# Performance work log

Measured on AMD Instinct MI355X. Metric: run time of the kernel, lower is better.

Reference implementation:

```python
import jax, jax.numpy as jnp
import numpy as np

K = 128      # knowledge_n
E = 4096     # exer_n
S = 2048     # student_n
M = 512      # number of supervised exercises (ex_id)
NUM_UPDATE = 3
THRESHOLD = 0.05
H = 1.0


def setup_inputs() -> dict:
    key = jax.random.key(0)
    ks = jax.random.split(key, 16)
    U_embeding = jax.random.uniform(ks[0], (S, K), dtype=jnp.float32)
    W = jax.random.uniform(ks[1], (K, E), dtype=jnp.float32)
    beiTa_1 = jax.random.uniform(ks[2], (K, E), dtype=jnp.float32)
    beiTa_2 = jax.random.uniform(ks[3], (E, 1), dtype=jnp.float32)
    B = jax.random.uniform(ks[4], (K, E, K), dtype=jnp.float32)
    guess_slip = jax.random.normal(ks[5], (E, 2), dtype=jnp.float32)
    A_emb = jax.random.normal(ks[6], (E, 3), dtype=jnp.float32)
    gamma_c = jax.random.normal(ks[7], (E, 1), dtype=jnp.float32)
    gamma_e = jax.random.normal(ks[8], (E, 1), dtype=jnp.float32)
    alpha = jax.random.normal(ks[9], (E, 1), dtype=jnp.float32)
    score = jax.random.randint(ks[10], (E, 1), 0, 2).astype(jnp.float32)
    user_k_kc = (jax.random.uniform(ks[11], (K, E)) < 0.3).astype(jnp.float32)
    # multi-hot question->concept map, ~4 concepts per exercise, at least 1
    q_kn = (jax.random.uniform(ks[12], (E, K)) < 4.0 / K).astype(jnp.float32)
    q_kn = q_kn.at[jnp.arange(E), jax.random.randint(ks[13], (E,), 0, K)].set(1.0)
    d = q_kn.sum(axis=1, keepdims=True)  # exercise degree, >= 1
    ex_id = jax.random.randint(ks[14], (M,), 0, E, dtype=jnp.int32)
    kn_id = jnp.arange(K, dtype=jnp.int32)
    stu_id = 7
    return dict(U_embeding=U_embeding, W=W, beiTa_1=beiTa_1, beiTa_2=beiTa_2,
                B=B, guess_slip=guess_slip, A_emb=A_emb, gamma_c=gamma_c,
                gamma_e=gamma_e, alpha=alpha, score=score, user_k_kc=user_k_kc,
                q_kn=q_kn, d=d, stu_id=stu_id, kn_id=kn_id, ex_id=ex_id)


def reference(U_embeding, W, beiTa_1, beiTa_2, B, guess_slip, A_emb,
              gamma_c, gamma_e, alpha, score, user_k_kc, q_kn, d,
              stu_id, kn_id, ex_id):
    # The torch loop `for cur_kn in kn_id: update(cur_kn, U_update[num-1])` is a
    # Jacobi sweep: every concept update reads the PREVIOUS state, so all
    # concepts can be computed in one vectorized pass per iteration.
    Bdiag = jnp.einsum('kek->ke', B)           # B[k, e, k], (K, E)
    dvec = d[:, 0]                              # (E,)
    sc = score[:, 0]                            # (E,)
    upd = jnp.zeros((K,), dtype=bool).at[kn_id].set(True)

    def step(u):                                # u: (K,) current mastery state
        # ---- Ic (eq. 7): per-exercise interaction term ----
        su = q_kn @ u                           # (E,)  sum of mastered concepts
        yc = jnp.exp(-(sc - su / dvec) ** 2)    # (E,)
        Pc = jnp.concatenate([1.0 - guess_slip, yc[:, None]], axis=1)  # (E,3)
        Ic = jax.nn.sigmoid(-jnp.sum(A_emb * Pc, axis=1))              # (E,)
        # ---- Gkc: masked, dead-zoned neighbour influence ----
        # U_gkc entries with q_kn==0 are set to 0.5, and column cur_kn is
        # zeroed; dead-zone of 0.5 contributes 0, so it reduces to a gated
        # product with the k-diagonal term subtracted out.
        dv = jnp.where(jnp.abs(u - 0.5) > THRESHOLD, u - 0.5, 0.0)      # (K,)
        qdv = q_kn * dv                         # (E, K)
        Gsum = jnp.einsum('kej,ej->ke', B, qdv) - Bdiag * qdv.T         # (K, E)
        # NOTE: the original subtracts 0.5 twice (sigmoid(...) - 0.5 then
        # reshape(...) - 0.5); replicated faithfully.
        Gkc = jax.nn.sigmoid(-Gsum) - 1.0       # (K, E)
        # ---- Zc ----
        Zc = jax.nn.sigmoid(-(gamma_c[:, 0] / dvec) * (sc - 0.5)) - 0.5  # (E,)
        # ---- WKC and the per-concept contraction over the exercise set ----
        WK = H * Ic[None, :] * (beiTa_1 * Gkc + (beiTa_2[:, 0] * Zc)[None, :])
        s = jnp.sum(user_k_kc * W * WK, axis=1)  # ragged set via 0/1 mask, (K,)
        u_new = jax.nn.sigmoid(-s)
        return jnp.where(upd, u_new, u)

    u0 = U_embeding[stu_id]                     # (K,)
    states = [u0]
    diffs = []
    for _ in range(NUM_UPDATE):
        un = step(states[-1])
        diffs.append(jnp.linalg.norm(un - states[-1]))
        states.append(un)

    state_last = states[-1][:, None]            # U_update[-2] in torch indexing
    state_2nd_last = states[-2][:, None]        # U_update[-3]
    diff_norm = jnp.stack(diffs)

    # ---- supervised predict ----
    Ukse = (q_kn[ex_id] @ state_last) / d[ex_id] - 0.5                  # (M,1)
    predict = jax.nn.sigmoid(-(alpha[ex_id] * Ukse + gamma_e[ex_id]))   # (M,1)
    return (state_last, state_2nd_last, predict, diff_norm)
```

## Files before the change

kernel.cpp:

```cpp
#include <hip/hip_runtime.h>
#include <math.h>

#define KK 128
#define EE 4096
#define MM 512
#define MAXNZ 32

#define OFF_PART 128
#define OFF_CNT  2176
#define OFF_IDX  6272
#define OFF_PE   137344

__global__ __launch_bounds__(256) void k_setup(
    const float* __restrict__ U, const float* __restrict__ beiTa_2,
    const float* __restrict__ guess_slip, const float* __restrict__ A_emb,
    const float* __restrict__ gamma_c, const float* __restrict__ score,
    const float* __restrict__ q_kn, const float* __restrict__ d,
    const int* __restrict__ stu_id, float* __restrict__ ws)
{
    int e = blockIdx.x * 256 + threadIdx.x;
    int* cnt = (int*)(ws + OFF_CNT);
    int* idx = (int*)(ws + OFF_IDX);
    float* P01  = ws + OFF_PE;
    float* a2   = P01 + EE;
    float* scv  = a2 + EE;
    float* invd = scv + EE;
    float* bz   = invd + EE;

    const float4* qrow = (const float4*)(q_kn + (size_t)e * KK);
    int c = 0;
    for (int j4 = 0; j4 < KK / 4; j4++) {
        float4 q = qrow[j4];
        int j = j4 * 4;
        if (q.x > 0.5f) { if (c < MAXNZ) idx[e * MAXNZ + c] = j;     c++; }
        if (q.y > 0.5f) { if (c < MAXNZ) idx[e * MAXNZ + c] = j + 1; c++; }
        if (q.z > 0.5f) { if (c < MAXNZ) idx[e * MAXNZ + c] = j + 2; c++; }
        if (q.w > 0.5f) { if (c < MAXNZ) idx[e * MAXNZ + c] = j + 3; c++; }
    }
    cnt[e] = (c < MAXNZ) ? c : MAXNZ;

    float id_ = 1.0f / d[e];
    invd[e] = id_;
    float scr = score[e];
    scv[e] = scr;
    P01[e] = A_emb[3 * e] * (1.0f - guess_slip[2 * e]) +
             A_emb[3 * e + 1] * (1.0f - guess_slip[2 * e + 1]);
    a2[e] = A_emb[3 * e + 2];
    float zc = 1.0f / (1.0f + __expf(gamma_c[e] * id_ * (scr - 0.5f))) - 0.5f;
    bz[e] = beiTa_2[e] * zc;

    if (blockIdx.x == 0 && threadIdx.x < KK) {
        ws[threadIdx.x] = U[(size_t)stu_id[0] * KK + threadIdx.x];
    }
}

__global__ __launch_bounds__(256) void k_iter(
    const float* __restrict__ B, const float* __restrict__ W,
    const float* __restrict__ beiTa_1, const float* __restrict__ ukc,
    float* __restrict__ ws)
{
    __shared__ float lu[KK];
    __shared__ float ldv[KK];
    __shared__ float red[256];
    int tid = threadIdx.x;
    int k = blockIdx.y;
    int e = blockIdx.x * 256 + tid;

    if (tid < KK) {
        float uv = ws[tid];
        lu[tid] = uv;
        float t = uv - 0.5f;
        ldv[tid] = (fabsf(t) > 0.05f) ? t : 0.0f;
    }
    __syncthreads();

    const int* cnt = (const int*)(ws + OFF_CNT);
    const int* ip  = (const int*)(ws + OFF_IDX) + e * MAXNZ;
    const float* P01  = ws + OFF_PE;
    const float* a2   = P01 + EE;
    const float* scv  = a2 + EE;
    const float* invd = scv + EE;
    const float* bz   = invd + EE;

    int c = cnt[e];
    const float* Brow = B + ((size_t)k * EE + (size_t)e) * KK;
    float su = 0.0f, gs = 0.0f;
    for (int i = 0; i < c; i++) {
        int j = ip[i];
        su += lu[j];
        float dvj = ldv[j];
        if (j != k && dvj != 0.0f) gs += Brow[j] * dvj;
    }
    float t0 = scv[e] - su * invd[e];
    float yc = __expf(-t0 * t0);
    float Ic  = 1.0f / (1.0f + __expf(P01[e] + a2[e] * yc));
    float Gkc = 1.0f / (1.0f + __expf(gs)) - 1.0f;
    size_t o = (size_t)k * EE + (size_t)e;
    float WKv = Ic * (beiTa_1[o] * Gkc + bz[e]);
    float contrib = ukc[o] * W[o] * WKv;

    red[tid] = contrib;
    __syncthreads();
    for (int s2 = 128; s2 > 0; s2 >>= 1) {
        if (tid < s2) red[tid] += red[tid + s2];
        __syncthreads();
    }
    if (tid == 0) ws[OFF_PART + k * 16 + blockIdx.x] = red[0];
}

__global__ __launch_bounds__(128) void k_update(float* __restrict__ ws,
                                                float* __restrict__ out, int iter)
{
    __shared__ float red[KK];
    int k = threadIdx.x;
    float s = 0.0f;
    for (int t = 0; t < 16; t++) s += ws[OFF_PART + k * 16 + t];
    float un = 1.0f / (1.0f + __expf(s));
    float uo = ws[k];
    float dd = un - uo;
    red[k] = dd * dd;
    __syncthreads();
    for (int s2 = 64; s2 > 0; s2 >>= 1) {
        if (k < s2) red[k] += red[k + s2];
        __syncthreads();
    }
    if (k == 0) out[768 + iter] = sqrtf(red[0]);
    ws[k] = un;
    if (iter == 1) out[128 + k] = un;
}

__global__ __launch_bounds__(512) void k_final(
    float* __restrict__ ws, float* __restrict__ out,
    const int* __restrict__ ex_id, const float* __restrict__ alpha,
    const float* __restrict__ gamma_e)
{
    __shared__ float un_s[KK];
    __shared__ float red[KK];
    int tid = threadIdx.x;
    if (tid < KK) {
        float s = 0.0f;
        for (int t = 0; t < 16; t++) s += ws[OFF_PART + tid * 16 + t];
        float un = 1.0f / (1.0f + __expf(s));
        float uo = ws[tid];
        float dd = un - uo;
        red[tid] = dd * dd;
        un_s[tid] = un;
        out[tid] = un;
    }
    __syncthreads();
    for (int s2 = 64; s2 > 0; s2 >>= 1) {
        if (tid < s2) red[tid] += red[tid + s2];
        __syncthreads();
    }
    if (tid == 0) out[770] = sqrtf(red[0]);

    const int* cnt = (const int*)(ws + OFF_CNT);
    const int* idx = (const int*)(ws + OFF_IDX);
    const float* invd = ws + OFF_PE + 3 * EE;
    int e = ex_id[tid];
    int c = cnt[e];
    const int* ip = idx + e * MAXNZ;
    float su = 0.0f;
    for (int i = 0; i < c; i++) su += un_s[ip[i]];
    float Ukse = su * invd[e] - 0.5f;
    float p = 1.0f / (1.0f + __expf(alpha[e] * Ukse + gamma_e[e]));
    out[256 + tid] = p;
}

extern "C" void kernel_launch(void* const* d_in, const int* in_sizes, int n_in,
                              void* d_out, int out_size, void* d_ws, size_t ws_size,
                              hipStream_t stream) {
    const float* U          = (const float*)d_in[0];
    const float* W          = (const float*)d_in[1];
    const float* beiTa_1    = (const float*)d_in[2];
    const float* beiTa_2    = (const float*)d_in[3];
    const float* B          = (const float*)d_in[4];
    const float* guess_slip = (const float*)d_in[5];
    const float* A_emb      = (const float*)d_in[6];
    const float* gamma_c    = (const float*)d_in[7];
    const float* gamma_e    = (const float*)d_in[8];
    const float* alpha      = (const float*)d_in[9];
    const float* score      = (const float*)d_in[10];
    const float* ukc        = (const float*)d_in[11];
    const float* q_kn       = (const float*)d_in[12];
    const float* d          = (const float*)d_in[13];
    const int*   stu_id     = (const int*)d_in[14];
    const int*   ex_id      = (const int*)d_in[16];
    float* out = (float*)d_out;
    float* ws  = (float*)d_ws;

    k_setup<<<16, 256, 0, stream>>>(U, beiTa_2, guess_slip, A_emb, gamma_c,
                                    score, q_kn, d, stu_id, ws);
    for (int iter = 0; iter < 3; iter++) {
        k_iter<<<dim3(16, 128), 256, 0, stream>>>(B, W, beiTa_1, ukc, ws);
        if (iter < 2) {
            k_update<<<1, 128, 0, stream>>>(ws, out, iter);
        } else {
            k_final<<<1, 512, 0, stream>>>(ws, out, ex_id, alpha, gamma_e);
        }
    }
}
```

Measured before the change: 500.6 us.

## Compact sparse B entries once, then run later sweeps on compacted transposed data

Result: slower. 698.3 us (+39.5%).

```diff
diff --git a/kernel.cpp b/kernel.cpp
--- a/kernel.cpp
+++ b/kernel.cpp
@@ -4,129 +4,244 @@
 #define KK 128
 #define EE 4096
 #define MM 512
-#define MAXNZ 32
-
-#define OFF_PART 128
-#define OFF_CNT  2176
-#define OFF_IDX  6272
-#define OFF_PE   137344
+#define CP 32
+
+#define OFF_U    0
+#define OFF_P0   128
+#define OFF_P1   (128 + 4096)
+#define OFF_CNT  20608
+#define OFF_IDX  24704
+#define OFF_PE   155776
+#define OFF_UWT  180352
+#define OFF_B1T  704640
+#define OFF_BC   1228928
 
 __global__ __launch_bounds__(256) void k_setup(
-    const float* __restrict__ U, const float* __restrict__ beiTa_2,
+    const float* __restrict__ U, const float* __restrict__ W,
+    const float* __restrict__ beiTa_1, const float* __restrict__ beiTa_2,
     const float* __restrict__ guess_slip, const float* __restrict__ A_emb,
     const float* __restrict__ gamma_c, const float* __restrict__ score,
-    const float* __restrict__ q_kn, const float* __restrict__ d,
-    const int* __restrict__ stu_id, float* __restrict__ ws)
-{
-    int e = blockIdx.x * 256 + threadIdx.x;
-    int* cnt = (int*)(ws + OFF_CNT);
-    int* idx = (int*)(ws + OFF_IDX);
-    float* P01  = ws + OFF_PE;
-    float* a2   = P01 + EE;
-    float* scv  = a2 + EE;
-    float* invd = scv + EE;
-    float* bz   = invd + EE;
-
-    const float4* qrow = (const float4*)(q_kn + (size_t)e * KK);
-    int c = 0;
-    for (int j4 = 0; j4 < KK / 4; j4++) {
-        float4 q = qrow[j4];
-        int j = j4 * 4;
-        if (q.x > 0.5f) { if (c < MAXNZ) idx[e * MAXNZ + c] = j;     c++; }
-        if (q.y > 0.5f) { if (c < MAXNZ) idx[e * MAXNZ + c] = j + 1; c++; }
-        if (q.z > 0.5f) { if (c < MAXNZ) idx[e * MAXNZ + c] = j + 2; c++; }
-        if (q.w > 0.5f) { if (c < MAXNZ) idx[e * MAXNZ + c] = j + 3; c++; }
-    }
-    cnt[e] = (c < MAXNZ) ? c : MAXNZ;
-
-    float id_ = 1.0f / d[e];
-    invd[e] = id_;
-    float scr = score[e];
-    scv[e] = scr;
-    P01[e] = A_emb[3 * e] * (1.0f - guess_slip[2 * e]) +
-             A_emb[3 * e + 1] * (1.0f - guess_slip[2 * e + 1]);
-    a2[e] = A_emb[3 * e + 2];
-    float zc = 1.0f / (1.0f + __expf(gamma_c[e] * id_ * (scr - 0.5f))) - 0.5f;
-    bz[e] = beiTa_2[e] * zc;
-
-    if (blockIdx.x == 0 && threadIdx.x < KK) {
-        ws[threadIdx.x] = U[(size_t)stu_id[0] * KK + threadIdx.x];
-    }
-}
-
-__global__ __launch_bounds__(256) void k_iter(
-    const float* __restrict__ B, const float* __restrict__ W,
-    const float* __restrict__ beiTa_1, const float* __restrict__ ukc,
+    const float* __restrict__ ukc, const float* __restrict__ q_kn,
+    const float* __restrict__ d, const int* __restrict__ stu_id,
     float* __restrict__ ws)
 {
-    __shared__ float lu[KK];
-    __shared__ float ldv[KK];
-    __shared__ float red[256];
-    int tid = threadIdx.x;
-    int k = blockIdx.y;
-    int e = blockIdx.x * 256 + tid;
-
+    int tid = threadIdx.x;
+    int blk = blockIdx.x;
+    if (blk < 16) {
+        int e = blk * 256 + tid;
+        int* cnt = (int*)(ws + OFF_CNT);
+        int* idx = (int*)(ws + OFF_IDX);
+        float* P01  = ws + OFF_PE;
+        float* a2   = P01 + EE;
+        float* scv  = a2 + EE;
+        float* invd = scv + EE;
+        float* bz   = invd + EE;
+        float* Icv  = bz + EE;
+
+        const float4* qrow = (const float4*)(q_kn + (size_t)e * KK);
+        int c = 0;
+        for (int j4 = 0; j4 < KK / 4; j4++) {
+            float4 q = qrow[j4];
+            int j = j4 * 4;
+            if (q.x > 0.5f) { if (c < CP) idx[e * CP + c] = j;     c++; }
+            if (q.y > 0.5f) { if (c < CP) idx[e * CP + c] = j + 1; c++; }
+            if (q.z > 0.5f) { if (c < CP) idx[e * CP + c] = j + 2; c++; }
+            if (q.w > 0.5f) { if (c < CP) idx[e * CP + c] = j + 3; c++; }
+        }
+        c = (c < CP) ? c : CP;
+        cnt[e] = c;
+
+        float id_ = 1.0f / d[e];
+        invd[e] = id_;
+        float scr = score[e];
+        scv[e] = scr;
+        float p01 = A_emb[3 * e] * (1.0f - guess_slip[2 * e]) +
+                    A_emb[3 * e + 1] * (1.0f - guess_slip[2 * e + 1]);
+        P01[e] = p01;
+        float a2v = A_emb[3 * e + 2];
+        a2[e] = a2v;
+        float zc = 1.0f / (1.0f + __expf(gamma_c[e] * id_ * (scr - 0.5f))) - 0.5f;
+        bz[e] = beiTa_2[e] * zc;
+
+        const float* u0p = U + (size_t)stu_id[0] * KK;
+        float su = 0.0f;
+        for (int i = 0; i < c; i++) su += u0p[idx[e * CP + i]];
+        float t0 = scr - su * id_;
+        float yc = __expf(-t0 * t0);
+        Icv[e] = 1.0f / (1.0f + __expf(p01 + a2v * yc));
+
+        if (blk == 0 && tid < KK) ws[tid] = u0p[tid];
+    } else {
+        float* uWt = ws + OFF_UWT;
+        float* b1t = ws + OFF_B1T;
+        for (int t = (blk - 16) * 256 + tid; t < KK * EE; t += 48 * 256) {
+            int e = t >> 7;
+            int k = t & (KK - 1);
+            size_t src = (size_t)k * EE + e;
+            uWt[t] = ukc[src] * W[src];
+            b1t[t] = beiTa_1[src];
+        }
+    }
+}
+
+__global__ __launch_bounds__(256) void k_dense(
+    const float* __restrict__ B, const float* __restrict__ q_kn,
+    const float* __restrict__ W, const float* __restrict__ beiTa_1,
+    const float* __restrict__ ukc, float* __restrict__ ws)
+{
+    __shared__ float sdv[KK];
+    int tid = threadIdx.x;
     if (tid < KK) {
         float uv = ws[tid];
-        lu[tid] = uv;
         float t = uv - 0.5f;
-        ldv[tid] = (fabsf(t) > 0.05f) ? t : 0.0f;
-    }
-    __syncthreads();
+        sdv[tid] = (fabsf(t) > 0.05f) ? t : 0.0f;
+    }
+    __syncthreads();
+
+    int w    = blockIdx.x * 4 + (tid >> 6);
+    int lane = tid & 63;
+    int k    = w >> 5;
+    int ec   = w & 31;
+    int half = lane >> 5;
+    int ll   = lane & 31;
+    int j0   = ll * 4;
+
+    float dvm0 = (j0     != k) ? sdv[j0]     : 0.0f;
+    float dvm1 = (j0 + 1 != k) ? sdv[j0 + 1] : 0.0f;
+    float dvm2 = (j0 + 2 != k) ? sdv[j0 + 2] : 0.0f;
+    float dvm3 = (j0 + 3 != k) ? sdv[j0 + 3] : 0.0f;
+
+    const float* bzv = ws + OFF_PE + 4 * EE;
+    const float* Icv = ws + OFF_PE + 5 * EE;
+    float* Bc = ws + OFF_BC;
+    unsigned long long Lmask = (ll ? ((1ull << ll) - 1ull) : 0ull) << (half * 32);
+
+    float acc = 0.0f;
+    int ebase = ec * 128;
+    for (int ee = 0; ee < 128; ee += 2) {
+        int e = ebase + ee + half;
+        const float4 bq = *(const float4*)(q_kn + (size_t)e * KK + j0);
+        const float4 bb = *(const float4*)(B + ((size_t)k * EE + e) * KK + j0);
+
+        float p = bb.x * (bq.x * dvm0) + bb.y * (bq.y * dvm1) +
+                  bb.z * (bq.z * dvm2) + bb.w * (bq.w * dvm3);
+
+        bool f0 = bq.x > 0.5f, f1 = bq.y > 0.5f, f2 = bq.z > 0.5f, f3 = bq.w > 0.5f;
+        unsigned long long m0 = __ballot(f0), m1 = __ballot(f1);
+        unsigned long long m2 = __ballot(f2), m3 = __ballot(f3);
+        int i0 = __popcll(m0 & Lmask) + __popcll(m1 & Lmask) +
+                 __popcll(m2 & Lmask) + __popcll(m3 & Lmask);
+        int i1 = i0 + (f0 ? 1 : 0);
+        int i2 = i1 + (f1 ? 1 : 0);
+        int i3 = i2 + (f2 ? 1 : 0);
+        size_t bcb = (size_t)e * CP * KK + k;
+        if (f0 && i0 < CP) Bc[bcb + (size_t)i0 * KK] = bb.x;
+        if (f1 && i1 < CP) Bc[bcb + (size_t)i1 * KK] = bb.y;
+        if (f2 && i2 < CP) Bc[bcb + (size_t)i2 * KK] = bb.z;
+        if (f3 && i3 < CP) Bc[bcb + (size_t)i3 * KK] = bb.w;
+
+        for (int m = 1; m <= 16; m <<= 1) p += __shfl_xor(p, m, 32);
+
+        if (ll == 0) {
+            float Gkc = 1.0f / (1.0f + __expf(p)) - 1.0f;
+            size_t o = (size_t)k * EE + e;
+            float WKv = Icv[e] * (beiTa_1[o] * Gkc + bzv[e]);
+            acc += ukc[o] * W[o] * WKv;
+        }
+    }
+    acc += __shfl_xor(acc, 32);
+    if (lane == 0) ws[OFF_P0 + k * 32 + ec] = acc;
+}
+
+__global__ __launch_bounds__(512) void k_update(float* __restrict__ ws,
+                                                float* __restrict__ out, int iter)
+{
+    __shared__ float un_s[KK];
+    __shared__ float red[KK];
+    int tid = threadIdx.x;
+    if (tid < KK) {
+        float s = 0.0f;
+        if (iter == 0) {
+            const float* p = ws + OFF_P0 + tid * 32;
+            for (int t = 0; t < 32; t++) s += p[t];
+        } else {
+            const float* p = ws + OFF_P1 + tid * 128;
+            for (int t = 0; t < 128; t++) s += p[t];
+        }
+        float un = 1.0f / (1.0f + __expf(s));
+        float uo = ws[tid];
+        float dd = un - uo;
+        red[tid] = dd * dd;
+        un_s[tid] = un;
+        ws[tid] = un;
+        if (iter == 1) out[128 + tid] = un;
+    }
+    __syncthreads();
+    for (int s2 = 64; s2 > 0; s2 >>= 1) {
+        if (tid < s2) red[tid] += red[tid + s2];
+        __syncthreads();
+    }
+    if (tid == 0) out[768 + iter] = sqrtf(red[0]);
 
     const int* cnt = (const int*)(ws + OFF_CNT);
-    const int* ip  = (const int*)(ws + OFF_IDX) + e * MAXNZ;
+    const int* idx = (const int*)(ws + OFF_IDX);
     const float* P01  = ws + OFF_PE;
     const float* a2   = P01 + EE;
     const float* scv  = a2 + EE;
     const float* invd = scv + EE;
-    const float* bz   = invd + EE;
-
-    int c = cnt[e];
-    const float* Brow = B + ((size_t)k * EE + (size_t)e) * KK;
-    float su = 0.0f, gs = 0.0f;
-    for (int i = 0; i < c; i++) {
-        int j = ip[i];
-        su += lu[j];
-        float dvj = ldv[j];
-        if (j != k && dvj != 0.0f) gs += Brow[j] * dvj;
-    }
-    float t0 = scv[e] - su * invd[e];
-    float yc = __expf(-t0 * t0);
-    float Ic  = 1.0f / (1.0f + __expf(P01[e] + a2[e] * yc));
-    float Gkc = 1.0f / (1.0f + __expf(gs)) - 1.0f;
-    size_t o = (size_t)k * EE + (size_t)e;
-    float WKv = Ic * (beiTa_1[o] * Gkc + bz[e]);
-    float contrib = ukc[o] * W[o] * WKv;
-
-    red[tid] = contrib;
-    __syncthreads();
-    for (int s2 = 128; s2 > 0; s2 >>= 1) {
-        if (tid < s2) red[tid] += red[tid + s2];
-        __syncthreads();
-    }
-    if (tid == 0) ws[OFF_PART + k * 16 + blockIdx.x] = red[0];
-}
-
-__global__ __launch_bounds__(128) void k_update(float* __restrict__ ws,
-                                                float* __restrict__ out, int iter)
-{
-    __shared__ float red[KK];
-    int k = threadIdx.x;
-    float s = 0.0f;
-    for (int t = 0; t < 16; t++) s += ws[OFF_PART + k * 16 + t];
-    float un = 1.0f / (1.0f + __expf(s));
-    float uo = ws[k];
-    float dd = un - uo;
-    red[k] = dd * dd;
-    __syncthreads();
-    for (int s2 = 64; s2 > 0; s2 >>= 1) {
-        if (k < s2) red[k] += red[k + s2];
-        __syncthreads();
-    }
-    if (k == 0) out[768 + iter] = sqrtf(red[0]);
-    ws[k] = un;
-    if (iter == 1) out[128 + k] = un;
+    float* Icv = ws + OFF_PE + 5 * EE;
+    for (int e = tid; e < EE; e += 512) {
+        int c = cnt[e];
+        const int* ip = idx + e * CP;
+        float su = 0.0f;
+        for (int i = 0; i < c; i++) su += un_s[ip[i]];
+        float t0 = scv[e] - su * invd[e];
+        float yc = __expf(-t0 * t0);
+        Icv[e] = 1.0f / (1.0f + __expf(P01[e] + a2[e] * yc));
+    }
+}
+
+__global__ __launch_bounds__(256) void k_sparse(float* __restrict__ ws)
+{
+    __shared__ float sdv[KK];
+    __shared__ float hacc[KK];
+    int tid = threadIdx.x;
+    int k = tid & (KK - 1);
+    int eh = tid >> 7;
+    if (tid < KK) {
+        float uv = ws[tid];
+        float t = uv - 0.5f;
+        sdv[tid] = (fabsf(t) > 0.05f) ? t : 0.0f;
+    }
+    __syncthreads();
+
+    const int* cnt = (const int*)(ws + OFF_CNT);
+    const int* idx = (const int*)(ws + OFF_IDX);
+    const float* bzv = ws + OFF_PE + 4 * EE;
+    const float* Icv = ws + OFF_PE + 5 * EE;
+    const float* uWt = ws + OFF_UWT;
+    const float* b1t = ws + OFF_B1T;
+    const float* Bc  = ws + OFF_BC;
+
+    float acc = 0.0f;
+    int ebase = blockIdx.x * 32;
+    for (int ee = 0; ee < 32; ee += 2) {
+        int e = ebase + ee + eh;
+        int c = cnt[e];
+        const int* ip = idx + e * CP;
+        const float* bp = Bc + (size_t)e * CP * KK + k;
+        float gs = 0.0f;
+        for (int i = 0; i < c; i++) {
+            int j = ip[i];
+            float b = bp[(size_t)i * KK];
+            gs += (j != k) ? b * sdv[j] : 0.0f;
+        }
+        float Gkc = 1.0f / (1.0f + __expf(gs)) - 1.0f;
+        acc += uWt[e * KK + k] * Icv[e] * (b1t[e * KK + k] * Gkc + bzv[e]);
+    }
+    if (eh == 1) hacc[k] = acc;
+    __syncthreads();
+    if (eh == 0) ws[OFF_P1 + k * 128 + blockIdx.x] = acc + hacc[k];
 }
 
 __global__ __launch_bounds__(512) void k_final(
@@ -139,7 +254,8 @@
     int tid = threadIdx.x;
     if (tid < KK) {
         float s = 0.0f;
-        for (int t = 0; t < 16; t++) s += ws[OFF_PART + tid * 16 + t];
+        const float* p = ws + OFF_P1 + tid * 128;
+        for (int t = 0; t < 128; t++) s += p[t];
         float un = 1.0f / (1.0f + __expf(s));
         float uo = ws[tid];
         float dd = un - uo;
@@ -159,12 +275,11 @@
     const float* invd = ws + OFF_PE + 3 * EE;
     int e = ex_id[tid];
     int c = cnt[e];
-    const int* ip = idx + e * MAXNZ;
+    const int* ip = idx + e * CP;
     float su = 0.0f;
     for (int i = 0; i < c; i++) su += un_s[ip[i]];
     float Ukse = su * invd[e] - 0.5f;
-    float p = 1.0f / (1.0f + __expf(alpha[e] * Ukse + gamma_e[e]));
-    out[256 + tid] = p;
+    out[256 + tid] = 1.0f / (1.0f + __expf(alpha[e] * Ukse + gamma_e[e]));
 }
 
 extern "C" void kernel_launch(void* const* d_in, const int* in_sizes, int n_in,
@@ -189,14 +304,12 @@
     float* out = (float*)d_out;
     float* ws  = (float*)d_ws;
 
-    k_setup<<<16, 256, 0, stream>>>(U, beiTa_2, guess_slip, A_emb, gamma_c,
-                                    score, q_kn, d, stu_id, ws);
-    for (int iter = 0; iter < 3; iter++) {
-        k_iter<<<dim3(16, 128), 256, 0, stream>>>(B, W, beiTa_1, ukc, ws);
-        if (iter < 2) {
-            k_update<<<1, 128, 0, stream>>>(ws, out, iter);
-        } else {
-            k_final<<<1, 512, 0, stream>>>(ws, out, ex_id, alpha, gamma_e);
-        }
-    }
-}
+    k_setup<<<64, 256, 0, stream>>>(U, W, beiTa_1, beiTa_2, guess_slip, A_emb,
+                                    gamma_c, score, ukc, q_kn, d, stu_id, ws);
+    k_dense<<<1024, 256, 0, stream>>>(B, q_kn, W, beiTa_1, ukc, ws);
+    k_update<<<1, 512, 0, stream>>>(ws, out, 0);
+    k_sparse<<<128, 256, 0, stream>>>(ws);
+    k_update<<<1, 512, 0, stream>>>(ws, out, 1);
+    k_sparse<<<128, 256, 0, stream>>>(ws);
+    k_final<<<1, 512, 0, stream>>>(ws, out, ex_id, alpha, gamma_e);
+}
```

## Compact sparse B entries once and stream them coalesced across iterations

Applied to the files above, without the earlier changes.

Result: no change. 493.0 us (-1.5%).

```diff
diff --git a/kernel.cpp b/kernel.cpp
--- a/kernel.cpp
+++ b/kernel.cpp
@@ -4,100 +4,149 @@
 #define KK 128
 #define EE 4096
 #define MM 512
-#define MAXNZ 32
-
-#define OFF_PART 128
+#define CP 32
+
+#define OFF_U    0
+#define OFF_P    128
 #define OFF_CNT  2176
 #define OFF_IDX  6272
-#define OFF_PE   137344
+#define OFF_IDXT 137344
+#define OFF_PE   268416
+#define OFF_GW   288896
+#define OFF_HW   813184
+#define OFF_BC   1337472
 
 __global__ __launch_bounds__(256) void k_setup(
-    const float* __restrict__ U, const float* __restrict__ beiTa_2,
+    const float* __restrict__ U, const float* __restrict__ W,
+    const float* __restrict__ beiTa_1, const float* __restrict__ beiTa_2,
     const float* __restrict__ guess_slip, const float* __restrict__ A_emb,
     const float* __restrict__ gamma_c, const float* __restrict__ score,
-    const float* __restrict__ q_kn, const float* __restrict__ d,
-    const int* __restrict__ stu_id, float* __restrict__ ws)
-{
-    int e = blockIdx.x * 256 + threadIdx.x;
-    int* cnt = (int*)(ws + OFF_CNT);
-    int* idx = (int*)(ws + OFF_IDX);
-    float* P01  = ws + OFF_PE;
-    float* a2   = P01 + EE;
-    float* scv  = a2 + EE;
-    float* invd = scv + EE;
-    float* bz   = invd + EE;
-
-    const float4* qrow = (const float4*)(q_kn + (size_t)e * KK);
-    int c = 0;
-    for (int j4 = 0; j4 < KK / 4; j4++) {
-        float4 q = qrow[j4];
-        int j = j4 * 4;
-        if (q.x > 0.5f) { if (c < MAXNZ) idx[e * MAXNZ + c] = j;     c++; }
-        if (q.y > 0.5f) { if (c < MAXNZ) idx[e * MAXNZ + c] = j + 1; c++; }
-        if (q.z > 0.5f) { if (c < MAXNZ) idx[e * MAXNZ + c] = j + 2; c++; }
-        if (q.w > 0.5f) { if (c < MAXNZ) idx[e * MAXNZ + c] = j + 3; c++; }
-    }
-    cnt[e] = (c < MAXNZ) ? c : MAXNZ;
-
-    float id_ = 1.0f / d[e];
-    invd[e] = id_;
-    float scr = score[e];
-    scv[e] = scr;
-    P01[e] = A_emb[3 * e] * (1.0f - guess_slip[2 * e]) +
-             A_emb[3 * e + 1] * (1.0f - guess_slip[2 * e + 1]);
-    a2[e] = A_emb[3 * e + 2];
-    float zc = 1.0f / (1.0f + __expf(gamma_c[e] * id_ * (scr - 0.5f))) - 0.5f;
-    bz[e] = beiTa_2[e] * zc;
-
-    if (blockIdx.x == 0 && threadIdx.x < KK) {
-        ws[threadIdx.x] = U[(size_t)stu_id[0] * KK + threadIdx.x];
-    }
-}
-
-__global__ __launch_bounds__(256) void k_iter(
-    const float* __restrict__ B, const float* __restrict__ W,
-    const float* __restrict__ beiTa_1, const float* __restrict__ ukc,
+    const float* __restrict__ ukc, const float* __restrict__ q_kn,
+    const float* __restrict__ d, const int* __restrict__ stu_id,
     float* __restrict__ ws)
 {
+    int tid = threadIdx.x;
+    int blk = blockIdx.x;
+    if (blk < 16) {
+        int e = blk * 256 + tid;
+        int* cnt  = (int*)(ws + OFF_CNT);
+        int* idx  = (int*)(ws + OFF_IDX);
+        int* idxT = (int*)(ws + OFF_IDXT);
+        float* P01  = ws + OFF_PE;
+        float* a2   = P01 + EE;
+        float* scv  = a2 + EE;
+        float* invd = scv + EE;
+        float* bz   = invd + EE;
+
+        int4 s4 = make_int4(255, 255, 255, 255);
+        for (int i4 = 0; i4 < CP / 4; i4++) ((int4*)(idx + e * CP))[i4] = s4;
+        const float4* qrow = (const float4*)(q_kn + (size_t)e * KK);
+        int c = 0;
+        for (int j4 = 0; j4 < KK / 4; j4++) {
+            float4 q = qrow[j4];
+            int j = j4 * 4;
+            if (q.x > 0.5f) { if (c < CP) { idx[e*CP+c] = j;   idxT[c*EE+e] = j;   } c++; }
+            if (q.y > 0.5f) { if (c < CP) { idx[e*CP+c] = j+1; idxT[c*EE+e] = j+1; } c++; }
+            if (q.z > 0.5f) { if (c < CP) { idx[e*CP+c] = j+2; idxT[c*EE+e] = j+2; } c++; }
+            if (q.w > 0.5f) { if (c < CP) { idx[e*CP+c] = j+3; idxT[c*EE+e] = j+3; } c++; }
+        }
+        c = (c < CP) ? c : CP;
+        cnt[e] = c;
+
+        float id_ = 1.0f / d[e];
+        invd[e] = id_;
+        float scr = score[e];
+        scv[e] = scr;
+        P01[e] = A_emb[3*e] * (1.0f - guess_slip[2*e]) +
+                 A_emb[3*e+1] * (1.0f - guess_slip[2*e+1]);
+        a2[e] = A_emb[3*e+2];
+        float zc = 1.0f / (1.0f + __expf(gamma_c[e] * id_ * (scr - 0.5f))) - 0.5f;
+        bz[e] = beiTa_2[e] * zc;
+
+        if (blk == 0 && tid < KK) ws[tid] = U[(size_t)stu_id[0] * KK + tid];
+    } else {
+        float* gW = ws + OFF_GW;
+        float* hW = ws + OFF_HW;
+        int stride = (gridDim.x - 16) * 256;
+        for (int t = (blk - 16) * 256 + tid; t < KK * EE; t += stride) {
+            float uw = ukc[t] * W[t];
+            hW[t] = uw;
+            gW[t] = uw * beiTa_1[t];
+        }
+    }
+}
+
+__global__ __launch_bounds__(256) void k_compact(const float* __restrict__ B,
+                                                 float* __restrict__ ws)
+{
+    __shared__ float srow[4][KK];
+    int tid  = threadIdx.x;
+    int wid  = tid >> 6;
+    int lane = tid & 63;
+    int w  = blockIdx.x * 4 + wid;
+    int k  = w >> 5;
+    int ec = w & 31;
+    const int* idx = (const int*)(ws + OFF_IDX);
+    float* Bc = ws + OFF_BC;
+    float* sr = srow[wid];
+
+    int ebase = ec * 128;
+    const float2* Brow = (const float2*)(B + ((size_t)k * EE + ebase) * KK);
+    for (int t = 0; t < 128; t++) {
+        int e = ebase + t;
+        float2 v = Brow[(size_t)t * (KK / 2) + lane];
+        int j = (lane < CP) ? idx[e * CP + lane] : 255;
+        ((float2*)sr)[lane] = v;
+        if (j < KK) {
+            float val = sr[j];
+            Bc[((size_t)k * CP + lane) * EE + e] = val;
+        }
+    }
+}
+
+__global__ __launch_bounds__(256) void k_sparse(float* __restrict__ ws)
+{
     __shared__ float lu[KK];
-    __shared__ float ldv[KK];
+    __shared__ float sdv[KK];
     __shared__ float red[256];
     int tid = threadIdx.x;
-    int k = blockIdx.y;
-    int e = blockIdx.x * 256 + tid;
+    int ec = blockIdx.x;
+    int k  = blockIdx.y;
+    int e  = ec * 256 + tid;
 
     if (tid < KK) {
         float uv = ws[tid];
         lu[tid] = uv;
         float t = uv - 0.5f;
-        ldv[tid] = (fabsf(t) > 0.05f) ? t : 0.0f;
-    }
-    __syncthreads();
-
-    const int* cnt = (const int*)(ws + OFF_CNT);
-    const int* ip  = (const int*)(ws + OFF_IDX) + e * MAXNZ;
+        sdv[tid] = (fabsf(t) > 0.05f) ? t : 0.0f;
+    }
+    __syncthreads();
+
+    const int* cnt    = (const int*)(ws + OFF_CNT);
+    const int* idxT   = (const int*)(ws + OFF_IDXT);
     const float* P01  = ws + OFF_PE;
     const float* a2   = P01 + EE;
     const float* scv  = a2 + EE;
     const float* invd = scv + EE;
-    const float* bz   = invd + EE;
+    const float* bzv  = invd + EE;
+    const float* gW   = ws + OFF_GW;
+    const float* hW   = ws + OFF_HW;
+    const float* Bc   = ws + OFF_BC;
 
     int c = cnt[e];
-    const float* Brow = B + ((size_t)k * EE + (size_t)e) * KK;
     float su = 0.0f, gs = 0.0f;
     for (int i = 0; i < c; i++) {
-        int j = ip[i];
+        int j   = idxT[i * EE + e];
+        float b = Bc[((size_t)k * CP + i) * EE + e];
         su += lu[j];
-        float dvj = ldv[j];
-        if (j != k && dvj != 0.0f) gs += Brow[j] * dvj;
+        gs += (j != k) ? b * sdv[j] : 0.0f;
     }
     float t0 = scv[e] - su * invd[e];
     float yc = __expf(-t0 * t0);
-    float Ic  = 1.0f / (1.0f + __expf(P01[e] + a2[e] * yc));
+    float Ic = 1.0f / (1.0f + __expf(P01[e] + a2[e] * yc));
     float Gkc = 1.0f / (1.0f + __expf(gs)) - 1.0f;
-    size_t o = (size_t)k * EE + (size_t)e;
-    float WKv = Ic * (beiTa_1[o] * Gkc + bz[e]);
-    float contrib = ukc[o] * W[o] * WKv;
+    size_t o = (size_t)k * EE + e;
+    float contrib = Ic * (gW[o] * Gkc + hW[o] * bzv[e]);
 
     red[tid] = contrib;
     __syncthreads();
@@ -105,7 +154,7 @@
         if (tid < s2) red[tid] += red[tid + s2];
         __syncthreads();
     }
-    if (tid == 0) ws[OFF_PART + k * 16 + blockIdx.x] = red[0];
+    if (tid == 0) ws[OFF_P + k * 16 + ec] = red[0];
 }
 
 __global__ __launch_bounds__(128) void k_update(float* __restrict__ ws,
@@ -114,7 +163,8 @@
     __shared__ float red[KK];
     int k = threadIdx.x;
     float s = 0.0f;
-    for (int t = 0; t < 16; t++) s += ws[OFF_PART + k * 16 + t];
+    const float* p = ws + OFF_P + k * 16;
+    for (int t = 0; t < 16; t++) s += p[t];
     float un = 1.0f / (1.0f + __expf(s));
     float uo = ws[k];
     float dd = un - uo;
@@ -139,7 +189,8 @@
     int tid = threadIdx.x;
     if (tid < KK) {
         float s = 0.0f;
-        for (int t = 0; t < 16; t++) s += ws[OFF_PART + tid * 16 + t];
+        const float* p = ws + OFF_P + tid * 16;
+        for (int t = 0; t < 16; t++) s += p[t];
         float un = 1.0f / (1.0f + __expf(s));
         float uo = ws[tid];
         float dd = un - uo;
@@ -159,12 +210,11 @@
     const float* invd = ws + OFF_PE + 3 * EE;
     int e = ex_id[tid];
     int c = cnt[e];
-    const int* ip = idx + e * MAXNZ;
+    const int* ip = idx + e * CP;
     float su = 0.0f;
     for (int i = 0; i < c; i++) su += un_s[ip[i]];
     float Ukse = su * invd[e] - 0.5f;
-    float p = 1.0f / (1.0f + __expf(alpha[e] * Ukse + gamma_e[e]));
-    out[256 + tid] = p;
+    out[256 + tid] = 1.0f / (1.0f + __expf(alpha[e] * Ukse + gamma_e[e]));
 }
 
 extern "C" void kernel_launch(void* const* d_in, const int* in_sizes, int n_in,
@@ -189,14 +239,13 @@
     float* out = (float*)d_out;
     float* ws  = (float*)d_ws;
 
-    k_setup<<<16, 256, 0, stream>>>(U, beiTa_2, guess_slip, A_emb, gamma_c,
-                                    score, q_kn, d, stu_id, ws);
-    for (int iter = 0; iter < 3; iter++) {
-        k_iter<<<dim3(16, 128), 256, 0, stream>>>(B, W, beiTa_1, ukc, ws);
-        if (iter < 2) {
-            k_update<<<1, 128, 0, stream>>>(ws, out, iter);
-        } else {
-            k_final<<<1, 512, 0, stream>>>(ws, out, ex_id, alpha, gamma_e);
-        }
-    }
-}
+    k_setup<<<144, 256, 0, stream>>>(U, W, beiTa_1, beiTa_2, guess_slip, A_emb,
+                                     gamma_c, score, ukc, q_kn, d, stu_id, ws);
+    k_compact<<<1024, 256, 0, stream>>>(B, ws);
+    k_sparse<<<dim3(16, 128), 256, 0, stream>>>(ws);
+    k_update<<<1, 128, 0, stream>>>(ws, out, 0);
+    k_sparse<<<dim3(16, 128), 256, 0, stream>>>(ws);
+    k_update<<<1, 128, 0, stream>>>(ws, out, 1);
+    k_sparse<<<dim3(16, 128), 256, 0, stream>>>(ws);
+    k_final<<<1, 512, 0, stream>>>(ws, out, ex_id, alpha, gamma_e);
+}
```
